# Kernel optimization log

Measured on AMD Instinct MI355X. Metric: run time of the kernel, lower is better.

Reference implementation:

```python
import jax, jax.numpy as jnp
import numpy as np

NEG = -1e20

def _rope(x):
    # x: (N, L, H, D). Original buffers use inv_freq over D with D/2 entries;
    # sin/cos tiled to full D to broadcast (original code's einsum was under-specified for 4D).
    L, D = x.shape[1], x.shape[3]
    inv_freq = 1.0 / (10000.0 ** (jnp.arange(0, D, 2, dtype=jnp.float32) / D))
    t = jnp.arange(L, dtype=jnp.float32)
    freqs = t[:, None] * inv_freq[None, :]            # (L, D/2)
    sin = jnp.concatenate([jnp.sin(freqs)] * 2, -1)[None, :, None, :]  # (1,L,1,D)
    cos = jnp.concatenate([jnp.cos(freqs)] * 2, -1)[None, :, None, :]
    return x * cos + jnp.flip(x, -1) * sin

def setup_inputs() -> dict:
    key = jax.random.key(0)
    ks = jax.random.split(key, 8)
    N, L, E, H = 2, 1024, 2048, 16
    D = E // H
    s = 0.02
    return {
        "values": jax.random.normal(ks[0], (N, L, E), jnp.float32),
        "keys": jax.random.normal(ks[1], (N, L, E), jnp.float32),
        "queries": jax.random.normal(ks[2], (N, L, E), jnp.float32),
        "mask": jax.random.randint(ks[3], (N, 1, L, L), 0, 2, jnp.int32),
        "Wv": jax.random.normal(ks[4], (D, D), jnp.float32) * s,
        "Wk": jax.random.normal(ks[5], (D, D), jnp.float32) * s,
        "Wq": jax.random.normal(ks[6], (D, D), jnp.float32) * s,
        "Wo": jax.random.normal(ks[7], (E, E), jnp.float32) * s,
        "bo": jnp.zeros((E,), jnp.float32),
    }

def reference(values, keys, queries, mask, Wv, Wk, Wq, Wo, bo):
    N, L, E = queries.shape
    H = 16
    D = E // H
    v = values.reshape(N, L, H, D)
    k = keys.reshape(N, L, H, D)
    q = queries.reshape(N, L, H, D)
    q = _rope(q)
    k = _rope(k)
    # per-head linears (nn.Linear: x @ W.T)
    v = jnp.einsum('nlhd,od->nlho', v, Wv)
    k = jnp.einsum('nlhd,od->nlho', k, Wk)
    q = jnp.einsum('nlhd,od->nlho', q, Wq)
    energy = jnp.einsum('nqhd,nkhd->nhqk', q, k)
    energy = jnp.where(mask == 0, NEG, energy)
    attn = jax.nn.softmax(energy / jnp.sqrt(jnp.float32(E)), axis=3)
    out = jnp.einsum('nhqk,nkhd->nqhd', attn, v).reshape(N, L, E)
    return out @ Wo.T + bo
```

## Files before the change

kernel.cpp:

```cpp
#include <hip/hip_runtime.h>

#define LQ 1024
#define EMB 2048
#define NH 16
#define HD 128
#define RSCALE 0.022097086912079608f

typedef unsigned short u16x8 __attribute__((ext_vector_type(8)));
typedef __bf16 bf16x8 __attribute__((ext_vector_type(8)));
typedef float f32x4 __attribute__((ext_vector_type(4)));

typedef const __attribute__((address_space(1))) unsigned int* gas_t;
typedef __attribute__((address_space(3))) unsigned int* las_t;

__device__ __forceinline__ void glds16(const void* g, void* l){
  __builtin_amdgcn_global_load_lds((gas_t)g, (las_t)l, 16, 0, 0);
}
__device__ __forceinline__ unsigned short f2b(float f){
  unsigned int x = __float_as_uint(f);
  return (unsigned short)((x + 0x7fffu + ((x >> 16) & 1u)) >> 16);
}
__device__ __forceinline__ bf16x8 as_bf(u16x8 u){
  union { u16x8 u; bf16x8 b; } c; c.u = u; return c.b;
}

__global__ __launch_bounds__(256) void k_prep(const float* __restrict__ Wo,
                                              unsigned short* __restrict__ Wob,
                                              const int* __restrict__ M,
                                              unsigned long long* __restrict__ Mb){
  int bx = blockIdx.x, t = threadIdx.x;
  if (bx < 4096) {
    int i = (bx * 256 + t) * 4;
    float4 f = *(const float4*)&Wo[i];
    ushort4 u;
    u.x = f2b(f.x); u.y = f2b(f.y); u.z = f2b(f.z); u.w = f2b(f.w);
    *(ushort4*)&Wob[i] = u;
  } else {
    int w_idx = (bx - 4096) * 4 + (t >> 6);
    int lane = t & 63;
    int n = w_idx >> 14, row = (w_idx >> 4) & 1023, wc = w_idx & 15;
    int v = M[(size_t)n * (LQ * LQ) + (size_t)row * LQ + wc * 64 + lane];
    unsigned long long b = __ballot(v != 0);
    if (lane == 0) Mb[w_idx] = b;
  }
}

__global__ __launch_bounds__(256) void k_proj(
    const float* __restrict__ vals, const float* __restrict__ keys,
    const float* __restrict__ qrys,
    const float* __restrict__ Wv, const float* __restrict__ Wk,
    const float* __restrict__ Wq,
    unsigned short* __restrict__ vp, unsigned short* __restrict__ kp,
    unsigned short* __restrict__ qp)
{
  __shared__ unsigned short Xs[64 * 136];
  __shared__ unsigned short Ws[128 * 136];
  __shared__ float scC[4 * 128], scS[4 * 128];
  int t = threadIdx.x;
  int which = blockIdx.y;
  const float* X; const float* W; unsigned short* OUT; bool rope;
  if (which == 0)      { X = vals; W = Wv; OUT = vp; rope = false; }
  else if (which == 1) { X = keys; W = Wk; OUT = kp; rope = true;  }
  else                 { X = qrys; W = Wq; OUT = qp; rope = true;  }
  int m0 = blockIdx.x * 64;

  #pragma unroll
  for (int i = 0; i < 8; ++i) {
    int ci = t + 256 * i;
    int row = ci >> 4, ch = ci & 15;
    float4 a = *(const float4*)&W[row * 128 + ch * 8];
    float4 b = *(const float4*)&W[row * 128 + ch * 8 + 4];
    u16x8 u;
    u[0]=f2b(a.x); u[1]=f2b(a.y); u[2]=f2b(a.z); u[3]=f2b(a.w);
    u[4]=f2b(b.x); u[5]=f2b(b.y); u[6]=f2b(b.z); u[7]=f2b(b.w);
    *(u16x8*)&Ws[row * 136 + ch * 8] = u;
  }
  if (rope) {
    int l0 = (blockIdx.x * 4) & 1023;
    #pragma unroll
    for (int i = 0; i < 2; ++i) {
      int idx = t + 256 * i;
      int li = idx >> 7, d = idx & 127, j = d & 63;
      float inv = 1.0f / powf(10000.0f, (float)(2 * j) * 0.0078125f);
      float ang = (float)(l0 + li) * inv;
      scC[idx] = cosf(ang);
      scS[idx] = sinf(ang);
    }
  }
  __syncthreads();
  #pragma unroll
  for (int i = 0; i < 8; ++i) {
    int fi = t + 256 * i;
    int row = fi >> 5, dq = (fi & 31) * 4;
    int gr = m0 + row;
    float4 x = *(const float4*)&X[(size_t)gr * HD + dq];
    ushort4 u;
    if (rope) {
      int li = row >> 4;
      float4 xm = *(const float4*)&X[(size_t)gr * HD + (124 - dq)];
      float4 c  = *(const float4*)&scC[li * 128 + dq];
      float4 s  = *(const float4*)&scS[li * 128 + dq];
      u.x = f2b(x.x * c.x + xm.w * s.x);
      u.y = f2b(x.y * c.y + xm.z * s.y);
      u.z = f2b(x.z * c.z + xm.y * s.z);
      u.w = f2b(x.w * c.w + xm.x * s.w);
    } else {
      u.x = f2b(x.x); u.y = f2b(x.y); u.z = f2b(x.z); u.w = f2b(x.w);
    }
    *(ushort4*)&Xs[row * 136 + dq] = u;
  }
  __syncthreads();

  int w = t >> 6, lane = t & 63, quad = lane >> 4, n16 = lane & 15;
  f32x4 of[4][2];
  #pragma unroll
  for (int a = 0; a < 4; ++a)
    { of[a][0] = (f32x4){0.f,0.f,0.f,0.f}; of[a][1] = (f32x4){0.f,0.f,0.f,0.f}; }

  #pragma unroll
  for (int kd = 0; kd < 4; ++kd) {
    bf16x8 bfr[2];
    #pragma unroll
    for (int b2 = 0; b2 < 2; ++b2)
      bfr[b2] = as_bf(*(const u16x8*)&Ws[(w * 32 + b2 * 16 + n16) * 136 + kd * 32 + quad * 8]);
    #pragma unroll
    for (int a = 0; a < 4; ++a) {
      bf16x8 af = as_bf(*(const u16x8*)&Xs[(a * 16 + n16) * 136 + kd * 32 + quad * 8]);
      of[a][0] = __builtin_amdgcn_mfma_f32_16x16x32_bf16(af, bfr[0], of[a][0], 0, 0, 0);
      of[a][1] = __builtin_amdgcn_mfma_f32_16x16x32_bf16(af, bfr[1], of[a][1], 0, 0, 0);
    }
  }

  #pragma unroll
  for (int a = 0; a < 4; ++a) {
    #pragma unroll
    for (int b2 = 0; b2 < 2; ++b2) {
      #pragma unroll
      for (int r = 0; r < 4; ++r) {
        int m = m0 + a * 16 + quad * 4 + r;
        int n = m >> 14, l = (m >> 4) & 1023, h = m & 15;
        int o = w * 32 + b2 * 16 + n16;
        OUT[(((size_t)(n * NH + h)) * LQ + l) * HD + o] = f2b(of[a][b2][r]);
      }
    }
  }
}

__global__ __launch_bounds__(256) void k_vtrans(const unsigned short* __restrict__ vp,
                                                unsigned short* __restrict__ vt){
  __shared__ unsigned short Ls[64 * 136];
  int t = threadIdx.x;
  int l0 = blockIdx.x * 64;
  size_t base = (size_t)blockIdx.y * LQ * HD;
  #pragma unroll
  for (int i = 0; i < 4; ++i) {
    int ci = t + 256 * i;
    int row = ci >> 4, ch = ci & 15;
    *(u16x8*)&Ls[row * 136 + ch * 8] =
        *(const u16x8*)&vp[base + (size_t)(l0 + row) * HD + ch * 8];
  }
  __syncthreads();
  #pragma unroll
  for (int i = 0; i < 4; ++i) {
    int idx = t + 256 * i;
    int d = idx & 127, lc = idx >> 7;
    u16x8 pk;
    #pragma unroll
    for (int j = 0; j < 8; ++j) pk[j] = Ls[(lc * 8 + j) * 136 + d];
    *(u16x8*)&vt[base + (size_t)d * LQ + l0 + lc * 8] = pk;
  }
}

__global__ __launch_bounds__(256) void k_attn(
    const unsigned short* __restrict__ qp, const unsigned short* __restrict__ kp,
    const unsigned short* __restrict__ vt, const unsigned long long* __restrict__ Mb,
    unsigned short* __restrict__ ao)
{
  __shared__ unsigned short Ks[64 * 128];
  __shared__ unsigned short Vt[128 * 64];
  __shared__ unsigned short Ss[4 * 16 * 72];
  int t = threadIdx.x, w = t >> 6, lane = t & 63, quad = lane >> 4, n16 = lane & 15;
  int bh = blockIdx.y, nIdx = bh >> 4, h = bh & 15;
  int q0 = blockIdx.x * 64;
  size_t base = (size_t)bh * LQ * HD;
  const unsigned short* Q = qp + base;
  const unsigned short* K = kp + base;
  const unsigned short* V = vt + base;

  bf16x8 qf[4];
  #pragma unroll
  for (int kd = 0; kd < 4; ++kd)
    qf[kd] = as_bf(*(const u16x8*)&Q[(size_t)(q0 + w * 16 + n16) * HD + kd * 32 + quad * 8]);

  const unsigned long long* MbRow =
      Mb + ((size_t)nIdx * LQ + q0 + w * 16 + quad * 4) * 16;

  f32x4 of[8];
  #pragma unroll
  for (int c = 0; c < 8; ++c) of[c] = (f32x4){0.f, 0.f, 0.f, 0.f};
  float lp[4] = {0.f, 0.f, 0.f, 0.f};
  unsigned short* Ssw = Ss + w * 1152;
  int ub = (t & 192);

  for (int kt = 0; kt < 16; ++kt) {
    int k0 = kt * 64;
    __syncthreads();
    #pragma unroll
    for (int i = 0; i < 4; ++i) {
      int ci = t + 256 * i;
      int krow = ci >> 4, kslot = ci & 15, kch = kslot ^ (krow & 7);
      glds16(&K[(size_t)(k0 + krow) * HD + kch * 8], &Ks[(ub + 256 * i) * 8]);
      int vrow = ci >> 3, vslot = ci & 7, vch = vslot ^ (vrow & 7);
      glds16(&V[(size_t)vrow * LQ + k0 + vch * 8], &Vt[(ub + 256 * i) * 8]);
    }
    unsigned long long mw[4];
    #pragma unroll
    for (int r = 0; r < 4; ++r) mw[r] = MbRow[r * 16 + kt];
    __syncthreads();

    f32x4 sf[4];
    #pragma unroll
    for (int c = 0; c < 4; ++c) sf[c] = (f32x4){0.f, 0.f, 0.f, 0.f};
    #pragma unroll
    for (int kd = 0; kd < 4; ++kd) {
      #pragma unroll
      for (int c = 0; c < 4; ++c) {
        int slot = (kd * 4 + quad) ^ (n16 & 7);
        bf16x8 kv = as_bf(*(const u16x8*)&Ks[(c * 16 + n16) * 128 + slot * 8]);
        sf[c] = __builtin_amdgcn_mfma_f32_16x16x32_bf16(qf[kd], kv, sf[c], 0, 0, 0);
      }
    }
    #pragma unroll
    for (int r = 0; r < 4; ++r) {
      #pragma unroll
      for (int c = 0; c < 4; ++c) {
        int bit = (int)((mw[r] >> (c * 16 + n16)) & 1ull);
        float p = bit ? __expf(sf[c][r] * RSCALE) : 0.f;
        lp[r] += p;
        Ssw[(quad * 4 + r) * 72 + c * 16 + n16] = f2b(p);
      }
    }
    #pragma unroll
    for (int ks = 0; ks < 2; ++ks) {
      bf16x8 pa = as_bf(*(const u16x8*)&Ssw[n16 * 72 + ks * 32 + quad * 8]);
      #pragma unroll
      for (int c2 = 0; c2 < 8; ++c2) {
        int slot = (ks * 4 + quad) ^ (n16 & 7);
        bf16x8 vv = as_bf(*(const u16x8*)&Vt[(c2 * 16 + n16) * 64 + slot * 8]);
        of[c2] = __builtin_amdgcn_mfma_f32_16x16x32_bf16(pa, vv, of[c2], 0, 0, 0);
      }
    }
  }

  #pragma unroll
  for (int r = 0; r < 4; ++r) {
    float s = lp[r];
    #pragma unroll
    for (int off = 1; off < 16; off <<= 1) s += __shfl_xor(s, off, 16);
    lp[r] = 1.0f / fmaxf(s, 1e-30f);
  }
  #pragma unroll
  for (int c2 = 0; c2 < 8; ++c2) {
    #pragma unroll
    for (int r = 0; r < 4; ++r) {
      ao[((size_t)(nIdx * LQ + q0 + w * 16 + quad * 4 + r)) * EMB + h * HD + c2 * 16 + n16] =
          f2b(of[c2][r] * lp[r]);
    }
  }
}

__global__ __launch_bounds__(256) void k_outproj(
    const unsigned short* __restrict__ ao, const unsigned short* __restrict__ Wob,
    const float* __restrict__ bo, float* __restrict__ out)
{
  __shared__ unsigned short As[128 * 64];
  __shared__ unsigned short Bs[128 * 64];
  int t = threadIdx.x;
  int w = t >> 6, lane = t & 63, quad = lane >> 4, n16 = lane & 15;
  int wm = w >> 1, wo = w & 1;
  int m0 = blockIdx.x * 128, o0 = blockIdx.y * 128;
  int ub = (t & 192);

  f32x4 of[4][4];
  #pragma unroll
  for (int a = 0; a < 4; ++a)
    #pragma unroll
    for (int b = 0; b < 4; ++b) of[a][b] = (f32x4){0.f, 0.f, 0.f, 0.f};

  for (int k0 = 0; k0 < EMB; k0 += 64) {
    __syncthreads();
    #pragma unroll
    for (int i = 0; i < 4; ++i) {
      int ci = t + 256 * i;
      int row = ci >> 3, slot = ci & 7, ch = slot ^ (row & 7);
      glds16(&ao [(size_t)(m0 + row) * EMB + k0 + ch * 8], &As[(ub + 256 * i) * 8]);
      glds16(&Wob[(size_t)(o0 + row) * EMB + k0 + ch * 8], &Bs[(ub + 256 * i) * 8]);
    }
    __syncthreads();
    #pragma unroll
    for (int kd = 0; kd < 2; ++kd) {
      bf16x8 af[4], bf[4];
      #pragma unroll
      for (int a = 0; a < 4; ++a) {
        int row = wm * 64 + a * 16 + n16;
        int slot = (kd * 4 + quad) ^ (n16 & 7);
        af[a] = as_bf(*(const u16x8*)&As[row * 64 + slot * 8]);
      }
      #pragma unroll
      for (int b = 0; b < 4; ++b) {
        int row = wo * 64 + b * 16 + n16;
        int slot = (kd * 4 + quad) ^ (n16 & 7);
        bf[b] = as_bf(*(const u16x8*)&Bs[row * 64 + slot * 8]);
      }
      #pragma unroll
      for (int a = 0; a < 4; ++a)
        #pragma unroll
        for (int b = 0; b < 4; ++b)
          of[a][b] = __builtin_amdgcn_mfma_f32_16x16x32_bf16(af[a], bf[b], of[a][b], 0, 0, 0);
    }
  }

  float bb[4];
  #pragma unroll
  for (int b = 0; b < 4; ++b) bb[b] = bo[o0 + wo * 64 + b * 16 + n16];
  #pragma unroll
  for (int a = 0; a < 4; ++a) {
    #pragma unroll
    for (int b = 0; b < 4; ++b) {
      #pragma unroll
      for (int r = 0; r < 4; ++r) {
        out[(size_t)(m0 + wm * 64 + a * 16 + quad * 4 + r) * EMB
            + o0 + wo * 64 + b * 16 + n16] = of[a][b][r] + bb[b];
      }
    }
  }
}

extern "C" void kernel_launch(void* const* d_in, const int* in_sizes, int n_in,
                              void* d_out, int out_size, void* d_ws, size_t ws_size,
                              hipStream_t stream) {
  (void)in_sizes; (void)n_in; (void)out_size; (void)ws_size;
  const float* vals = (const float*)d_in[0];
  const float* keys = (const float*)d_in[1];
  const float* qrys = (const float*)d_in[2];
  const int*   mask = (const int*)d_in[3];
  const float* Wv   = (const float*)d_in[4];
  const float* Wk   = (const float*)d_in[5];
  const float* Wq   = (const float*)d_in[6];
  const float* Wo   = (const float*)d_in[7];
  const float* bo   = (const float*)d_in[8];
  float* out = (float*)d_out;

  unsigned short* U  = (unsigned short*)d_ws;
  unsigned short* qp = U;
  unsigned short* kp = U + 4194304;
  unsigned short* vp = U + 8388608;
  unsigned short* vt = U + 12582912;
  unsigned short* ao = U + 16777216;
  unsigned short* Wob= U + 20971520;
  unsigned long long* Mb = (unsigned long long*)(U + 25165824);

  k_prep    <<<dim3(12288),  dim3(256), 0, stream>>>(Wo, Wob, mask, Mb);
  k_proj    <<<dim3(512, 3), dim3(256), 0, stream>>>(vals, keys, qrys, Wv, Wk, Wq,
                                                     vp, kp, qp);
  k_vtrans  <<<dim3(16, 32), dim3(256), 0, stream>>>(vp, vt);
  k_attn    <<<dim3(16, 32), dim3(256), 0, stream>>>(qp, kp, vt, Mb, ao);
  k_outproj <<<dim3(16, 16), dim3(256), 0, stream>>>(ao, Wob, bo, out);
}
```

Measured before the change: 225.6 us.

## Double-buffer K/V and GEMM tiles, fold softmax scale into Q projection

The attention and output-projection kernels now keep two LDS buffers. The next K/V (or A/B) tile is prefetched with async global-to-LDS loads while MFMAs work on the current one, which removes one barrier per iteration and overlaps memory with compute. The softmax scale is folded into the Q projection epilogue, dropping a multiply from the inner loop. The per-wave score scratch gets a different row padding. Doubling LDS per block may lower occupancy, and scaling Q before the bf16 rounding slightly changes numerics.

```diff
diff --git a/kernel.cpp b/kernel.cpp
--- a/kernel.cpp
+++ b/kernel.cpp
@@ -62,6 +62,7 @@
   if (which == 0)      { X = vals; W = Wv; OUT = vp; rope = false; }
   else if (which == 1) { X = keys; W = Wk; OUT = kp; rope = true;  }
   else                 { X = qrys; W = Wq; OUT = qp; rope = true;  }
+  float qs = (which == 2) ? RSCALE : 1.0f;
   int m0 = blockIdx.x * 64;
 
   #pragma unroll
@@ -140,7 +141,7 @@
         int m = m0 + a * 16 + quad * 4 + r;
         int n = m >> 14, l = (m >> 4) & 1023, h = m & 15;
         int o = w * 32 + b2 * 16 + n16;
-        OUT[(((size_t)(n * NH + h)) * LQ + l) * HD + o] = f2b(of[a][b2][r]);
+        OUT[(((size_t)(n * NH + h)) * LQ + l) * HD + o] = f2b(of[a][b2][r] * qs);
       }
     }
   }
@@ -176,9 +177,9 @@
     const unsigned short* __restrict__ vt, const unsigned long long* __restrict__ Mb,
     unsigned short* __restrict__ ao)
 {
-  __shared__ unsigned short Ks[64 * 128];
-  __shared__ unsigned short Vt[128 * 64];
-  __shared__ unsigned short Ss[4 * 16 * 72];
+  __shared__ unsigned short Ks[2][64 * 128];
+  __shared__ unsigned short Vt[2][128 * 64];
+  __shared__ unsigned short Ss[4 * 16 * 76];
   int t = threadIdx.x, w = t >> 6, lane = t & 63, quad = lane >> 4, n16 = lane & 15;
   int bh = blockIdx.y, nIdx = bh >> 4, h = bh & 15;
   int q0 = blockIdx.x * 64;
@@ -199,24 +200,38 @@
   #pragma unroll
   for (int c = 0; c < 8; ++c) of[c] = (f32x4){0.f, 0.f, 0.f, 0.f};
   float lp[4] = {0.f, 0.f, 0.f, 0.f};
-  unsigned short* Ssw = Ss + w * 1152;
+  unsigned short* Ssw = Ss + w * 1216;
   int ub = (t & 192);
 
+  unsigned long long mw[4];
+  #pragma unroll
+  for (int r = 0; r < 4; ++r) mw[r] = MbRow[r * 16];
+  #pragma unroll
+  for (int i = 0; i < 4; ++i) {
+    int ci = t + 256 * i;
+    int krow = ci >> 4, kch = (ci & 15) ^ (krow & 7);
+    glds16(&K[(size_t)krow * HD + kch * 8], &Ks[0][(ub + 256 * i) * 8]);
+    int vrow = ci >> 3, vch = (ci & 7) ^ (vrow & 7);
+    glds16(&V[(size_t)vrow * LQ + vch * 8], &Vt[0][(ub + 256 * i) * 8]);
+  }
+
   for (int kt = 0; kt < 16; ++kt) {
-    int k0 = kt * 64;
+    int cur = kt & 1;
     __syncthreads();
-    #pragma unroll
-    for (int i = 0; i < 4; ++i) {
-      int ci = t + 256 * i;
-      int krow = ci >> 4, kslot = ci & 15, kch = kslot ^ (krow & 7);
-      glds16(&K[(size_t)(k0 + krow) * HD + kch * 8], &Ks[(ub + 256 * i) * 8]);
-      int vrow = ci >> 3, vslot = ci & 7, vch = vslot ^ (vrow & 7);
-      glds16(&V[(size_t)vrow * LQ + k0 + vch * 8], &Vt[(ub + 256 * i) * 8]);
-    }
-    unsigned long long mw[4];
-    #pragma unroll
-    for (int r = 0; r < 4; ++r) mw[r] = MbRow[r * 16 + kt];
-    __syncthreads();
+    unsigned long long mwn[4];
+    if (kt < 15) {
+      int k1 = (kt + 1) * 64;
+      #pragma unroll
+      for (int i = 0; i < 4; ++i) {
+        int ci = t + 256 * i;
+        int krow = ci >> 4, kch = (ci & 15) ^ (krow & 7);
+        glds16(&K[(size_t)(k1 + krow) * HD + kch * 8], &Ks[1 - cur][(ub + 256 * i) * 8]);
+        int vrow = ci >> 3, vch = (ci & 7) ^ (vrow & 7);
+        glds16(&V[(size_t)vrow * LQ + k1 + vch * 8], &Vt[1 - cur][(ub + 256 * i) * 8]);
+      }
+      #pragma unroll
+      for (int r = 0; r < 4; ++r) mwn[r] = MbRow[r * 16 + kt + 1];
+    }
 
     f32x4 sf[4];
     #pragma unroll
@@ -226,7 +241,7 @@
       #pragma unroll
       for (int c = 0; c < 4; ++c) {
         int slot = (kd * 4 + quad) ^ (n16 & 7);
-        bf16x8 kv = as_bf(*(const u16x8*)&Ks[(c * 16 + n16) * 128 + slot * 8]);
+        bf16x8 kv = as_bf(*(const u16x8*)&Ks[cur][(c * 16 + n16) * 128 + slot * 8]);
         sf[c] = __builtin_amdgcn_mfma_f32_16x16x32_bf16(qf[kd], kv, sf[c], 0, 0, 0);
       }
     }
@@ -235,21 +250,23 @@
       #pragma unroll
       for (int c = 0; c < 4; ++c) {
         int bit = (int)((mw[r] >> (c * 16 + n16)) & 1ull);
-        float p = bit ? __expf(sf[c][r] * RSCALE) : 0.f;
+        float p = bit ? __expf(sf[c][r]) : 0.f;
         lp[r] += p;
-        Ssw[(quad * 4 + r) * 72 + c * 16 + n16] = f2b(p);
+        Ssw[(quad * 4 + r) * 76 + c * 16 + n16] = f2b(p);
       }
     }
     #pragma unroll
     for (int ks = 0; ks < 2; ++ks) {
-      bf16x8 pa = as_bf(*(const u16x8*)&Ssw[n16 * 72 + ks * 32 + quad * 8]);
+      bf16x8 pa = as_bf(*(const u16x8*)&Ssw[n16 * 76 + ks * 32 + quad * 8]);
       #pragma unroll
       for (int c2 = 0; c2 < 8; ++c2) {
         int slot = (ks * 4 + quad) ^ (n16 & 7);
-        bf16x8 vv = as_bf(*(const u16x8*)&Vt[(c2 * 16 + n16) * 64 + slot * 8]);
+        bf16x8 vv = as_bf(*(const u16x8*)&Vt[cur][(c2 * 16 + n16) * 64 + slot * 8]);
         of[c2] = __builtin_amdgcn_mfma_f32_16x16x32_bf16(pa, vv, of[c2], 0, 0, 0);
       }
     }
+    #pragma unroll
+    for (int r = 0; r < 4; ++r) mw[r] = mwn[r];
   }
 
   #pragma unroll
@@ -273,8 +290,8 @@
     const unsigned short* __restrict__ ao, const unsigned short* __restrict__ Wob,
     const float* __restrict__ bo, float* __restrict__ out)
 {
-  __shared__ unsigned short As[128 * 64];
-  __shared__ unsigned short Bs[128 * 64];
+  __shared__ unsigned short As[2][128 * 64];
+  __shared__ unsigned short Bs[2][128 * 64];
   int t = threadIdx.x;
   int w = t >> 6, lane = t & 63, quad = lane >> 4, n16 = lane & 15;
   int wm = w >> 1, wo = w & 1;
@@ -287,30 +304,39 @@
     #pragma unroll
     for (int b = 0; b < 4; ++b) of[a][b] = (f32x4){0.f, 0.f, 0.f, 0.f};
 
-  for (int k0 = 0; k0 < EMB; k0 += 64) {
+  #pragma unroll
+  for (int i = 0; i < 4; ++i) {
+    int ci = t + 256 * i;
+    int row = ci >> 3, ch = (ci & 7) ^ (row & 7);
+    glds16(&ao [(size_t)(m0 + row) * EMB + ch * 8], &As[0][(ub + 256 * i) * 8]);
+    glds16(&Wob[(size_t)(o0 + row) * EMB + ch * 8], &Bs[0][(ub + 256 * i) * 8]);
+  }
+
+  for (int kt = 0; kt < 32; ++kt) {
+    int cur = kt & 1;
     __syncthreads();
-    #pragma unroll
-    for (int i = 0; i < 4; ++i) {
-      int ci = t + 256 * i;
-      int row = ci >> 3, slot = ci & 7, ch = slot ^ (row & 7);
-      glds16(&ao [(size_t)(m0 + row) * EMB + k0 + ch * 8], &As[(ub + 256 * i) * 8]);
-      glds16(&Wob[(size_t)(o0 + row) * EMB + k0 + ch * 8], &Bs[(ub + 256 * i) * 8]);
-    }
-    __syncthreads();
+    if (kt < 31) {
+      int k1 = (kt + 1) * 64;
+      #pragma unroll
+      for (int i = 0; i < 4; ++i) {
+        int ci = t + 256 * i;
+        int row = ci >> 3, ch = (ci & 7) ^ (row & 7);
+        glds16(&ao [(size_t)(m0 + row) * EMB + k1 + ch * 8], &As[1 - cur][(ub + 256 * i) * 8]);
+        glds16(&Wob[(size_t)(o0 + row) * EMB + k1 + ch * 8], &Bs[1 - cur][(ub + 256 * i) * 8]);
+      }
+    }
     #pragma unroll
     for (int kd = 0; kd < 2; ++kd) {
       bf16x8 af[4], bf[4];
       #pragma unroll
       for (int a = 0; a < 4; ++a) {
-        int row = wm * 64 + a * 16 + n16;
         int slot = (kd * 4 + quad) ^ (n16 & 7);
-        af[a] = as_bf(*(const u16x8*)&As[row * 64 + slot * 8]);
+        af[a] = as_bf(*(const u16x8*)&As[cur][(wm * 64 + a * 16 + n16) * 64 + slot * 8]);
       }
       #pragma unroll
       for (int b = 0; b < 4; ++b) {
-        int row = wo * 64 + b * 16 + n16;
         int slot = (kd * 4 + quad) ^ (n16 & 7);
-        bf[b] = as_bf(*(const u16x8*)&Bs[row * 64 + slot * 8]);
+        bf[b] = as_bf(*(const u16x8*)&Bs[cur][(wo * 64 + b * 16 + n16) * 64 + slot * 8]);
       }
       #pragma unroll
       for (int a = 0; a < 4; ++a)
```

New measurement: 227.1 us. No clear change (+0.7%).

## Keep softmax probabilities in registers, prescale Q, double-buffer out-projection tiles

Applied to the files above, without the earlier changes.

The attention kernel now computes the transposed score tile (K·Q), so each lane's probabilities line up with the A operand of a 16x16x16 bf16 MFMA. This removes the shared-memory round trip for P and the four per-row mask loads, and the softmax scale is folded into the Q projection. The output projection switches to 128x64 tiles with double-buffered LDS and a prefetch of the next K-slice, launching twice as many blocks. The risks are the smaller-K MFMA for the PV product, which issues more instructions, and an extra barrier for the row-sum reduction.

```diff
diff --git a/kernel.cpp b/kernel.cpp
--- a/kernel.cpp
+++ b/kernel.cpp
@@ -9,6 +9,7 @@
 typedef unsigned short u16x8 __attribute__((ext_vector_type(8)));
 typedef __bf16 bf16x8 __attribute__((ext_vector_type(8)));
 typedef float f32x4 __attribute__((ext_vector_type(4)));
+typedef short s16x4 __attribute__((ext_vector_type(4)));
 
 typedef const __attribute__((address_space(1))) unsigned int* gas_t;
 typedef __attribute__((address_space(3))) unsigned int* las_t;
@@ -22,6 +23,9 @@
 }
 __device__ __forceinline__ bf16x8 as_bf(u16x8 u){
   union { u16x8 u; bf16x8 b; } c; c.u = u; return c.b;
+}
+__device__ __forceinline__ f32x4 mfma16(s16x4 a, s16x4 b, f32x4 c){
+  return __builtin_amdgcn_mfma_f32_16x16x16bf16_1k(a, b, c, 0, 0, 0);
 }
 
 __global__ __launch_bounds__(256) void k_prep(const float* __restrict__ Wo,
@@ -62,6 +66,7 @@
   if (which == 0)      { X = vals; W = Wv; OUT = vp; rope = false; }
   else if (which == 1) { X = keys; W = Wk; OUT = kp; rope = true;  }
   else                 { X = qrys; W = Wq; OUT = qp; rope = true;  }
+  float qs = (which == 2) ? RSCALE : 1.0f;
   int m0 = blockIdx.x * 64;
 
   #pragma unroll
@@ -140,7 +145,7 @@
         int m = m0 + a * 16 + quad * 4 + r;
         int n = m >> 14, l = (m >> 4) & 1023, h = m & 15;
         int o = w * 32 + b2 * 16 + n16;
-        OUT[(((size_t)(n * NH + h)) * LQ + l) * HD + o] = f2b(of[a][b2][r]);
+        OUT[(((size_t)(n * NH + h)) * LQ + l) * HD + o] = f2b(of[a][b2][r] * qs);
       }
     }
   }
@@ -178,7 +183,7 @@
 {
   __shared__ unsigned short Ks[64 * 128];
   __shared__ unsigned short Vt[128 * 64];
-  __shared__ unsigned short Ss[4 * 16 * 72];
+  __shared__ float ls[4][16];
   int t = threadIdx.x, w = t >> 6, lane = t & 63, quad = lane >> 4, n16 = lane & 15;
   int bh = blockIdx.y, nIdx = bh >> 4, h = bh & 15;
   int q0 = blockIdx.x * 64;
@@ -193,13 +198,12 @@
     qf[kd] = as_bf(*(const u16x8*)&Q[(size_t)(q0 + w * 16 + n16) * HD + kd * 32 + quad * 8]);
 
   const unsigned long long* MbRow =
-      Mb + ((size_t)nIdx * LQ + q0 + w * 16 + quad * 4) * 16;
+      Mb + ((size_t)nIdx * LQ + q0 + w * 16 + n16) * 16;
 
   f32x4 of[8];
   #pragma unroll
   for (int c = 0; c < 8; ++c) of[c] = (f32x4){0.f, 0.f, 0.f, 0.f};
-  float lp[4] = {0.f, 0.f, 0.f, 0.f};
-  unsigned short* Ssw = Ss + w * 1152;
+  float lp = 0.f;
   int ub = (t & 192);
 
   for (int kt = 0; kt < 16; ++kt) {
@@ -208,14 +212,12 @@
     #pragma unroll
     for (int i = 0; i < 4; ++i) {
       int ci = t + 256 * i;
-      int krow = ci >> 4, kslot = ci & 15, kch = kslot ^ (krow & 7);
+      int krow = ci >> 4, kch = (ci & 15) ^ (krow & 7);
       glds16(&K[(size_t)(k0 + krow) * HD + kch * 8], &Ks[(ub + 256 * i) * 8]);
-      int vrow = ci >> 3, vslot = ci & 7, vch = vslot ^ (vrow & 7);
+      int vrow = ci >> 3, vch = (ci & 7) ^ (vrow & 7);
       glds16(&V[(size_t)vrow * LQ + k0 + vch * 8], &Vt[(ub + 256 * i) * 8]);
     }
-    unsigned long long mw[4];
-    #pragma unroll
-    for (int r = 0; r < 4; ++r) mw[r] = MbRow[r * 16 + kt];
+    unsigned long long mq = MbRow[kt];
     __syncthreads();
 
     f32x4 sf[4];
@@ -227,44 +229,47 @@
       for (int c = 0; c < 4; ++c) {
         int slot = (kd * 4 + quad) ^ (n16 & 7);
         bf16x8 kv = as_bf(*(const u16x8*)&Ks[(c * 16 + n16) * 128 + slot * 8]);
-        sf[c] = __builtin_amdgcn_mfma_f32_16x16x32_bf16(qf[kd], kv, sf[c], 0, 0, 0);
-      }
-    }
-    #pragma unroll
-    for (int r = 0; r < 4; ++r) {
-      #pragma unroll
-      for (int c = 0; c < 4; ++c) {
-        int bit = (int)((mw[r] >> (c * 16 + n16)) & 1ull);
-        float p = bit ? __expf(sf[c][r] * RSCALE) : 0.f;
-        lp[r] += p;
-        Ssw[(quad * 4 + r) * 72 + c * 16 + n16] = f2b(p);
-      }
-    }
-    #pragma unroll
-    for (int ks = 0; ks < 2; ++ks) {
-      bf16x8 pa = as_bf(*(const u16x8*)&Ssw[n16 * 72 + ks * 32 + quad * 8]);
+        sf[c] = __builtin_amdgcn_mfma_f32_16x16x32_bf16(kv, qf[kd], sf[c], 0, 0, 0);
+      }
+    }
+    #pragma unroll
+    for (int c = 0; c < 4; ++c) {
+      s16x4 pa;
+      #pragma unroll
+      for (int r = 0; r < 4; ++r) {
+        int bit = (int)((mq >> (c * 16 + quad * 4 + r)) & 1ull);
+        float p = bit ? __expf(sf[c][r]) : 0.f;
+        lp += p;
+        pa[r] = (short)f2b(p);
+      }
+      int cc = 2 * c + (quad >> 1);
       #pragma unroll
       for (int c2 = 0; c2 < 8; ++c2) {
-        int slot = (ks * 4 + quad) ^ (n16 & 7);
-        bf16x8 vv = as_bf(*(const u16x8*)&Vt[(c2 * 16 + n16) * 64 + slot * 8]);
-        of[c2] = __builtin_amdgcn_mfma_f32_16x16x32_bf16(pa, vv, of[c2], 0, 0, 0);
-      }
-    }
-  }
-
-  #pragma unroll
-  for (int r = 0; r < 4; ++r) {
-    float s = lp[r];
-    #pragma unroll
-    for (int off = 1; off < 16; off <<= 1) s += __shfl_xor(s, off, 16);
-    lp[r] = 1.0f / fmaxf(s, 1e-30f);
-  }
+        int row = c2 * 16 + n16;
+        int slot = cc ^ (n16 & 7);
+        s16x4 vv = *(const s16x4*)&Vt[row * 64 + slot * 8 + (quad & 1) * 4];
+        of[c2] = mfma16(pa, vv, of[c2]);
+      }
+    }
+  }
+
+  {
+    float s = lp;
+    s += __shfl_xor(s, 16);
+    s += __shfl_xor(s, 32);
+    ls[w][n16] = s;
+  }
+  __syncthreads();
+  float linv[4];
+  #pragma unroll
+  for (int r = 0; r < 4; ++r) linv[r] = 1.0f / fmaxf(ls[w][quad * 4 + r], 1e-30f);
+
   #pragma unroll
   for (int c2 = 0; c2 < 8; ++c2) {
     #pragma unroll
     for (int r = 0; r < 4; ++r) {
       ao[((size_t)(nIdx * LQ + q0 + w * 16 + quad * 4 + r)) * EMB + h * HD + c2 * 16 + n16] =
-          f2b(of[c2][r] * lp[r]);
+          f2b(of[c2][r] * linv[r]);
     }
   }
 }
@@ -273,64 +278,77 @@
     const unsigned short* __restrict__ ao, const unsigned short* __restrict__ Wob,
     const float* __restrict__ bo, float* __restrict__ out)
 {
-  __shared__ unsigned short As[128 * 64];
-  __shared__ unsigned short Bs[128 * 64];
+  __shared__ unsigned short As[2][128 * 64];
+  __shared__ unsigned short Bs[2][64 * 64];
   int t = threadIdx.x;
   int w = t >> 6, lane = t & 63, quad = lane >> 4, n16 = lane & 15;
   int wm = w >> 1, wo = w & 1;
-  int m0 = blockIdx.x * 128, o0 = blockIdx.y * 128;
+  int m0 = blockIdx.x * 128, o0 = blockIdx.y * 64;
   int ub = (t & 192);
 
-  f32x4 of[4][4];
+  f32x4 of[4][2];
   #pragma unroll
   for (int a = 0; a < 4; ++a)
-    #pragma unroll
-    for (int b = 0; b < 4; ++b) of[a][b] = (f32x4){0.f, 0.f, 0.f, 0.f};
-
-  for (int k0 = 0; k0 < EMB; k0 += 64) {
+    { of[a][0] = (f32x4){0.f,0.f,0.f,0.f}; of[a][1] = (f32x4){0.f,0.f,0.f,0.f}; }
+
+  #pragma unroll
+  for (int i = 0; i < 4; ++i) {
+    int ci = t + 256 * i;
+    int row = ci >> 3, ch = (ci & 7) ^ (row & 7);
+    glds16(&ao[(size_t)(m0 + row) * EMB + ch * 8], &As[0][(ub + 256 * i) * 8]);
+  }
+  #pragma unroll
+  for (int i = 0; i < 2; ++i) {
+    int ci = t + 256 * i;
+    int row = ci >> 3, ch = (ci & 7) ^ (row & 7);
+    glds16(&Wob[(size_t)(o0 + row) * EMB + ch * 8], &Bs[0][(ub + 256 * i) * 8]);
+  }
+
+  for (int kt = 0; kt < 32; ++kt) {
+    int cur = kt & 1;
     __syncthreads();
-    #pragma unroll
-    for (int i = 0; i < 4; ++i) {
-      int ci = t + 256 * i;
-      int row = ci >> 3, slot = ci & 7, ch = slot ^ (row & 7);
-      glds16(&ao [(size_t)(m0 + row) * EMB + k0 + ch * 8], &As[(ub + 256 * i) * 8]);
-      glds16(&Wob[(size_t)(o0 + row) * EMB + k0 + ch * 8], &Bs[(ub + 256 * i) * 8]);
-    }
-    __syncthreads();
+    if (kt < 31) {
+      int k1 = (kt + 1) * 64;
+      #pragma unroll
+      for (int i = 0; i < 4; ++i) {
+        int ci = t + 256 * i;
+        int row = ci >> 3, ch = (ci & 7) ^ (row & 7);
+        glds16(&ao[(size_t)(m0 + row) * EMB + k1 + ch * 8], &As[1 - cur][(ub + 256 * i) * 8]);
+      }
+      #pragma unroll
+      for (int i = 0; i < 2; ++i) {
+        int ci = t + 256 * i;
+        int row = ci >> 3, ch = (ci & 7) ^ (row & 7);
+        glds16(&Wob[(size_t)(o0 + row) * EMB + k1 + ch * 8], &Bs[1 - cur][(ub + 256 * i) * 8]);
+      }
+    }
     #pragma unroll
     for (int kd = 0; kd < 2; ++kd) {
-      bf16x8 af[4], bf[4];
-      #pragma unroll
-      for (int a = 0; a < 4; ++a) {
-        int row = wm * 64 + a * 16 + n16;
-        int slot = (kd * 4 + quad) ^ (n16 & 7);
-        af[a] = as_bf(*(const u16x8*)&As[row * 64 + slot * 8]);
-      }
-      #pragma unroll
-      for (int b = 0; b < 4; ++b) {
-        int row = wo * 64 + b * 16 + n16;
-        int slot = (kd * 4 + quad) ^ (n16 & 7);
-        bf[b] = as_bf(*(const u16x8*)&Bs[row * 64 + slot * 8]);
-      }
+      int slot0 = (kd * 4 + quad);
+      bf16x8 af[4], bf[2];
+      #pragma unroll
+      for (int a = 0; a < 4; ++a)
+        af[a] = as_bf(*(const u16x8*)&As[cur][(wm * 64 + a * 16 + n16) * 64 + (slot0 ^ (n16 & 7)) * 8]);
+      #pragma unroll
+      for (int b = 0; b < 2; ++b)
+        bf[b] = as_bf(*(const u16x8*)&Bs[cur][(wo * 32 + b * 16 + n16) * 64 + (slot0 ^ (n16 & 7)) * 8]);
       #pragma unroll
       for (int a = 0; a < 4; ++a)
         #pragma unroll
-        for (int b = 0; b < 4; ++b)
+        for (int b = 0; b < 2; ++b)
           of[a][b] = __builtin_amdgcn_mfma_f32_16x16x32_bf16(af[a], bf[b], of[a][b], 0, 0, 0);
     }
   }
 
-  float bb[4];
-  #pragma unroll
-  for (int b = 0; b < 4; ++b) bb[b] = bo[o0 + wo * 64 + b * 16 + n16];
+  float bb[2] = { bo[o0 + wo * 32 + n16], bo[o0 + wo * 32 + 16 + n16] };
   #pragma unroll
   for (int a = 0; a < 4; ++a) {
     #pragma unroll
-    for (int b = 0; b < 4; ++b) {
+    for (int b = 0; b < 2; ++b) {
       #pragma unroll
       for (int r = 0; r < 4; ++r) {
         out[(size_t)(m0 + wm * 64 + a * 16 + quad * 4 + r) * EMB
-            + o0 + wo * 64 + b * 16 + n16] = of[a][b][r] + bb[b];
+            + o0 + wo * 32 + b * 16 + n16] = of[a][b][r] + bb[b];
       }
     }
   }
@@ -365,5 +383,5 @@
                                                      vp, kp, qp);
   k_vtrans  <<<dim3(16, 32), dim3(256), 0, stream>>>(vp, vt);
   k_attn    <<<dim3(16, 32), dim3(256), 0, stream>>>(qp, kp, vt, Mb, ao);
-  k_outproj <<<dim3(16, 16), dim3(256), 0, stream>>>(ao, Wob, bo, out);
-}
+  k_outproj <<<dim3(16, 32), dim3(256), 0, stream>>>(ao, Wob, bo, out);
+}
```

After: 214.3 us. 5.0% less time.
